# Performance work log

Hardware: AMD Instinct MI355X
Metric: run time of the kernel (lower is better)

## Reference

```python
import jax, jax.numpy as jnp
import numpy as np

LMAX = 6
F_IN, F_OUT = 64, 64
N_ROT = 64  # n_angles**3
IRREP_FLAT = sum((2 * l + 1) ** 2 for l in range(LMAX + 1))  # 455
BATCH = 1024


def setup_inputs() -> dict:
    key = jax.random.key(0)
    k_x, k_d, k_w = jax.random.split(key, 3)
    x = jax.random.normal(k_x, (BATCH, F_IN, IRREP_FLAT), dtype=jnp.float32)
    D = jax.random.normal(k_d, (N_ROT, IRREP_FLAT), dtype=jnp.float32)  # flat Wigner-D buffer
    w = jax.random.normal(k_w, (F_IN, F_OUT, N_ROT), dtype=jnp.float32)
    return {"x": x, "D": D, "w": w}


def reference(x, D, w):
    B, f_in, _ = x.shape
    f_out = w.shape[1]
    n_rot = D.shape[0]
    # psi[f,g,i] = sum_n D[n,i] * w[f,g,n] / sqrt(N)
    psi = jnp.einsum('ni,fgn->fgi', D, w) / jnp.sqrt(jnp.asarray(n_rot, x.dtype))
    outs = []
    off = 0
    for l in range(LMAX + 1):
        d = 2 * l + 1          # irrep dim == multiplicity for so3_irreps
        blk = d * d
        # weight block: (f_in, f_out, mul_in=u, mul_out=v)
        Wl = psi[:, :, off:off + blk].reshape(f_in, f_out, d, d)
        # input block: (B, f_in, mul=u, irrep_dim=m)
        xl = x[:, :, off:off + blk].reshape(B, f_in, d, d)
        # e3nn Linear path norm ('element'): 1/sqrt(f_in * mul_in)
        norm = 1.0 / np.sqrt(f_in * d)
        yl = jnp.einsum('bfum,fguv->bgvm', xl, Wl) * norm
        outs.append(yl.reshape(B, f_out, blk))
        off += blk
    return jnp.concatenate(outs, axis=-1)  # (B, f_out, 455)
```

## Files before the change

kernel.cpp:

```cpp
#include <hip/hip_runtime.h>
#include <stdint.h>


typedef __bf16 bf16x8 __attribute__((ext_vector_type(8)));
typedef float floatx4 __attribute__((ext_vector_type(4)));

#define XROW 29120

__device__ __forceinline__ unsigned short f2bf(float f) {
  union { float f; unsigned int u; } c; c.f = f;
  unsigned int u = c.u;
  return (unsigned short)((u + 0x7FFFu + ((u >> 16) & 1u)) >> 16);
}
__device__ __forceinline__ unsigned int pack2(float a, float b) {
  return (unsigned int)f2bf(a) | ((unsigned int)f2bf(b) << 16);
}

__host__ __device__ constexpr int d_of(int L) { return 2 * L + 1; }
__host__ __device__ constexpr int off_of(int L) { int s = 0; for (int i = 0; i < L; ++i) s += d_of(i) * d_of(i); return s; }
__host__ __device__ constexpr size_t a_off(int L) { size_t s = 0; for (int i = 0; i < L; ++i) s += (size_t)65536 * d_of(i) * d_of(i); return s; }
__host__ __device__ constexpr size_t b_off(int L) { size_t s = a_off(7); for (int i = 0; i < L; ++i) s += (size_t)4096 * d_of(i) * (d_of(i) + 1); return s; }

__global__ __launch_bounds__(256) void prep(const float* __restrict__ x, const float* __restrict__ Dm,
                                            const float* __restrict__ w, unsigned short* __restrict__ ws) {
  __shared__ __align__(16) float smem[64 * 68 + 64 * 172];
  const int tid = threadIdx.x;
  const int bid = blockIdx.x;

  if (bid < 448) {
    float* wg = smem;
    float* Dl = smem + 64 * 68;
    const int g = bid & 63, l = bid >> 6;
    const int d = 2 * l + 1, d2 = d * d, K = 64 * d;
    int off = 0; size_t boff = a_off(7);
    for (int i = 0; i < l; ++i) { int dd = 2 * i + 1; off += dd * dd; boff += (size_t)4096 * dd * (dd + 1); }
    unsigned short* B = ws + boff;

    for (int t = tid; t < 4096; t += 256) {
      int n = t & 63, f = t >> 6;
      wg[n * 68 + f] = w[(size_t)f * 4096 + g * 64 + n];
    }
    for (int t = tid; t < 64 * 172; t += 256) {
      int n = t / 172, r = t - n * 172;
      Dl[t] = (r < d2) ? Dm[n * 455 + off + r] : 0.f;
    }
    __syncthreads();

    const float sl = 1.0f / (64.0f * sqrtf((float)d));
    const int RT = (d2 + 3) >> 2;
    for (int tt = tid; tt < 16 * RT; tt += 256) {
      const int ft = tt & 15, rt = tt >> 4;
      float acc[4][4] = {};
      for (int n = 0; n < 64; ++n) {
        floatx4 wv = *(const floatx4*)(wg + n * 68 + ft * 4);
        floatx4 dv = *(const floatx4*)(Dl + n * 172 + rt * 4);
#pragma unroll
        for (int a = 0; a < 4; ++a)
#pragma unroll
          for (int b2 = 0; b2 < 4; ++b2) acc[a][b2] += wv[a] * dv[b2];
      }
#pragma unroll
      for (int b2 = 0; b2 < 4; ++b2) {
        int r = rt * 4 + b2;
        if (r < d2) {
          int u = r / d, v = r - u * d;
          size_t base = (size_t)(g * d + v) * K + u * 64 + ft * 4;
#pragma unroll
          for (int a = 0; a < 4; ++a) B[base + a] = f2bf(acc[a][b2] * sl);
        }
      }
    }
    {
      int nn = 64 * d + g;
      for (int k = tid; k < K; k += 256) B[(size_t)nn * K + k] = 0;
    }
  } else {
    float* xs = smem;
    const int b = bid - 448;
    const float* xb = x + (size_t)b * XROW;
    size_t aoff = 0;

    for (int t = tid; t < 64 * 165; t += 256) { int f = t / 165, c = t - f * 165; xs[t] = xb[(size_t)f * 455 + c]; }
    __syncthreads();
    int off = 0;
#pragma unroll
    for (int l = 0; l < 5; ++l) {
      const int d = 2 * l + 1, d2 = d * d, n1 = 64 * d2;
      unsigned int* A = (unsigned int*)(ws + aoff + (size_t)b * n1);
      for (int t = tid; t < (n1 >> 1); t += 256) {
        int f2 = t & 31, s = t >> 5;
        int u = s % d, m = s / d;
        int c = off + u * d + m;
        A[t] = pack2(xs[(2 * f2) * 165 + c], xs[(2 * f2 + 1) * 165 + c]);
      }
      off += d2; aoff += (size_t)1024 * n1;
    }
    __syncthreads();
    for (int t = tid; t < 64 * 121; t += 256) { int f = t / 121, c = t - f * 121; xs[t] = xb[(size_t)f * 455 + 165 + c]; }
    __syncthreads();
    {
      const int n1 = 64 * 121;
      unsigned int* A = (unsigned int*)(ws + aoff + (size_t)b * n1);
      for (int t = tid; t < (n1 >> 1); t += 256) {
        int f2 = t & 31, s = t >> 5;
        int u = s % 11, m = s / 11;
        int c = u * 11 + m;
        A[t] = pack2(xs[(2 * f2) * 121 + c], xs[(2 * f2 + 1) * 121 + c]);
      }
      aoff += (size_t)1024 * n1;
    }
    __syncthreads();
    for (int t = tid; t < 64 * 169; t += 256) { int f = t / 169, c = t - f * 169; xs[t] = xb[(size_t)f * 455 + 286 + c]; }
    __syncthreads();
    {
      const int n1 = 64 * 169;
      unsigned int* A = (unsigned int*)(ws + aoff + (size_t)b * n1);
      for (int t = tid; t < (n1 >> 1); t += 256) {
        int f2 = t & 31, s = t >> 5;
        int u = s % 13, m = s / 13;
        int c = u * 13 + m;
        A[t] = pack2(xs[(2 * f2) * 169 + c], xs[(2 * f2 + 1) * 169 + c]);
      }
    }
  }
}

__device__ __forceinline__ void async_copy16(const void* gp, void* lp) {
  __builtin_amdgcn_global_load_lds((__attribute__((address_space(1))) void*)gp,
                                   (__attribute__((address_space(3))) void*)lp, 16, 0, 0);
}

template <int L>
__device__ __forceinline__ void gemm_body(int local, const unsigned short* __restrict__ ws,
                                          float* __restrict__ out,
                                          unsigned short* As, unsigned short* Bs) {
  constexpr int d = 2 * L + 1;
  constexpr int K = 64 * d;
  constexpr int NT = (d + 1) / 2;
  constexpr int OFF = off_of(L);
  const unsigned short* A = ws + a_off(L);
  const unsigned short* B = ws + b_off(L);
  const int x8 = local & 7, tt = local >> 3;
  const int mt = (tt / NT) * 8 + x8;
  const int nt = tt % NT;
  const int tid = threadIdx.x;
  const int w = tid >> 6, ln = tid & 63;
  const int wm = w >> 1, wn = w & 1;
  const int q = ln >> 4, r16 = ln & 15;

  const unsigned short* gp[4];
  unsigned short* ldst[4];
#pragma unroll
  for (int i = 0; i < 4; ++i) {
    int c = i * 256 + tid;
    if (i < 2) {
      gp[i] = A + (size_t)(mt * 128 + (c >> 2)) * K + (c & 3) * 8;
      ldst[i] = As + (i * 256 + w * 64) * 8;
    } else {
      int c2 = c - 512;
      gp[i] = B + (size_t)(nt * 128 + (c2 >> 2)) * K + (c2 & 3) * 8;
      ldst[i] = Bs + ((i - 2) * 256 + w * 64) * 8;
    }
  }

  const int aoffs0 = (wm * 64 + r16) * 32 + q * 8;
  const int boffs0 = (wn * 64 + r16) * 32 + q * 8;

  floatx4 acc[4][4] = {};

  for (int kt = 0; kt < 2 * d; ++kt) {
    __syncthreads();
#pragma unroll
    for (int i = 0; i < 4; ++i) async_copy16(gp[i], ldst[i]);
    __syncthreads();
    bf16x8 af[4], bfr[4];
#pragma unroll
    for (int mi = 0; mi < 4; ++mi) af[mi] = *(const bf16x8*)(As + aoffs0 + mi * 512);
#pragma unroll
    for (int ni = 0; ni < 4; ++ni) bfr[ni] = *(const bf16x8*)(Bs + boffs0 + ni * 512);
#pragma unroll
    for (int mi = 0; mi < 4; ++mi)
#pragma unroll
      for (int ni = 0; ni < 4; ++ni)
        acc[mi][ni] = __builtin_amdgcn_mfma_f32_16x16x32_bf16(af[mi], bfr[ni], acc[mi][ni], 0, 0, 0);
#pragma unroll
    for (int i = 0; i < 4; ++i) gp[i] += 32;
  }

#pragma unroll
  for (int ni = 0; ni < 4; ++ni) {
    int Cc = nt * 128 + wn * 64 + ni * 16 + r16;
    if (Cc < 64 * d) {
      int g = Cc / d, v = Cc - (Cc / d) * d;
#pragma unroll
      for (int mi = 0; mi < 4; ++mi) {
        int R0 = mt * 128 + wm * 64 + mi * 16 + q * 4;
#pragma unroll
        for (int reg = 0; reg < 4; ++reg) {
          int R = R0 + reg;
          int bb = R / d, m = R - (R / d) * d;
          out[(size_t)bb * XROW + g * 455 + OFF + v * d + m] = acc[mi][ni][reg];
        }
      }
    }
  }
}

__global__ __launch_bounds__(256) void gemm_all(const unsigned short* __restrict__ ws, float* __restrict__ out) {
  __shared__ alignas(16) unsigned short As[128 * 32];
  __shared__ alignas(16) unsigned short Bs[128 * 32];
  int b0 = 2015 - (int)blockIdx.x;
  if      (b0 <    8) gemm_body<0>(b0,        ws, out, As, Bs);
  else if (b0 <   56) gemm_body<1>(b0 -    8, ws, out, As, Bs);
  else if (b0 <  176) gemm_body<2>(b0 -   56, ws, out, As, Bs);
  else if (b0 <  400) gemm_body<3>(b0 -  176, ws, out, As, Bs);
  else if (b0 <  760) gemm_body<4>(b0 -  400, ws, out, As, Bs);
  else if (b0 < 1288) gemm_body<5>(b0 -  760, ws, out, As, Bs);
  else                gemm_body<6>(b0 - 1288, ws, out, As, Bs);
}

extern "C" void kernel_launch(void* const* d_in, const int* in_sizes, int n_in,
                              void* d_out, int out_size, void* d_ws, size_t ws_size,
                              hipStream_t stream) {
  const float* x = (const float*)d_in[0];
  const float* D = (const float*)d_in[1];
  const float* w = (const float*)d_in[2];
  float* out = (float*)d_out;
  unsigned short* ws = (unsigned short*)d_ws;

  hipLaunchKernelGGL(prep, dim3(1472), dim3(256), 0, stream, x, D, w, ws);
  hipLaunchKernelGGL(gemm_all, dim3(2016), dim3(256), 0, stream, ws, out);
}
```

Before: 364.5 us.

## Double-buffer LDS tiles in grouped GEMM and XOR-swizzle LDS layout

The GEMM main loop now keeps two LDS buffers for A and B, issuing the async global-to-LDS copy for the next k-tile before computing on the current one, with a single barrier per iteration instead of two. The 16-byte chunk index within each 64-byte row is XOR-swizzled on both the load and the read side to reduce LDS bank conflicts on the bf16x8 fragment reads. This doubles LDS use per block, which may lower occupancy, and correctness depends on the async copies having completed when the single barrier is passed.

```diff
diff --git a/kernel.cpp b/kernel.cpp
--- a/kernel.cpp
+++ b/kernel.cpp
@@ -138,6 +138,7 @@
   constexpr int K = 64 * d;
   constexpr int NT = (d + 1) / 2;
   constexpr int OFF = off_of(L);
+  constexpr int KT = 2 * d;
   const unsigned short* A = ws + a_off(L);
   const unsigned short* B = ws + b_off(L);
   const int x8 = local & 7, tt = local >> 3;
@@ -154,37 +155,48 @@
   for (int i = 0; i < 4; ++i) {
     int c = i * 256 + tid;
     if (i < 2) {
-      gp[i] = A + (size_t)(mt * 128 + (c >> 2)) * K + (c & 3) * 8;
+      int row = c >> 2, ch = (c & 3) ^ ((c >> 3) & 3);
+      gp[i] = A + (size_t)(mt * 128 + row) * K + ch * 8;
       ldst[i] = As + (i * 256 + w * 64) * 8;
     } else {
       int c2 = c - 512;
-      gp[i] = B + (size_t)(nt * 128 + (c2 >> 2)) * K + (c2 & 3) * 8;
+      int row = c2 >> 2, ch = (c2 & 3) ^ ((c2 >> 3) & 3);
+      gp[i] = B + (size_t)(nt * 128 + row) * K + ch * 8;
       ldst[i] = Bs + ((i - 2) * 256 + w * 64) * 8;
     }
   }
 
-  const int aoffs0 = (wm * 64 + r16) * 32 + q * 8;
-  const int boffs0 = (wn * 64 + r16) * 32 + q * 8;
+  const int sq = q ^ ((r16 >> 1) & 3);
+  const int aoffs0 = (wm * 64 + r16) * 32 + sq * 8;
+  const int boffs0 = (wn * 64 + r16) * 32 + sq * 8;
 
   floatx4 acc[4][4] = {};
 
-  for (int kt = 0; kt < 2 * d; ++kt) {
-    __syncthreads();
-#pragma unroll
-    for (int i = 0; i < 4; ++i) async_copy16(gp[i], ldst[i]);
-    __syncthreads();
+#pragma unroll
+  for (int i = 0; i < 4; ++i) { async_copy16(gp[i], ldst[i]); gp[i] += 32; }
+  __syncthreads();
+
+  int cur = 0;
+  for (int kt = 0; kt < KT; ++kt) {
+    if (kt + 1 < KT) {
+      const int nb = (cur ^ 1) * 4096;
+#pragma unroll
+      for (int i = 0; i < 4; ++i) { async_copy16(gp[i], ldst[i] + nb); gp[i] += 32; }
+    }
+    const unsigned short* Asc = As + cur * 4096;
+    const unsigned short* Bsc = Bs + cur * 4096;
     bf16x8 af[4], bfr[4];
 #pragma unroll
-    for (int mi = 0; mi < 4; ++mi) af[mi] = *(const bf16x8*)(As + aoffs0 + mi * 512);
-#pragma unroll
-    for (int ni = 0; ni < 4; ++ni) bfr[ni] = *(const bf16x8*)(Bs + boffs0 + ni * 512);
+    for (int mi = 0; mi < 4; ++mi) af[mi] = *(const bf16x8*)(Asc + aoffs0 + mi * 512);
+#pragma unroll
+    for (int ni = 0; ni < 4; ++ni) bfr[ni] = *(const bf16x8*)(Bsc + boffs0 + ni * 512);
 #pragma unroll
     for (int mi = 0; mi < 4; ++mi)
 #pragma unroll
       for (int ni = 0; ni < 4; ++ni)
         acc[mi][ni] = __builtin_amdgcn_mfma_f32_16x16x32_bf16(af[mi], bfr[ni], acc[mi][ni], 0, 0, 0);
-#pragma unroll
-    for (int i = 0; i < 4; ++i) gp[i] += 32;
+    __syncthreads();
+    cur ^= 1;
   }
 
 #pragma unroll
@@ -207,8 +219,8 @@
 }
 
 __global__ __launch_bounds__(256) void gemm_all(const unsigned short* __restrict__ ws, float* __restrict__ out) {
-  __shared__ alignas(16) unsigned short As[128 * 32];
-  __shared__ alignas(16) unsigned short Bs[128 * 32];
+  __shared__ alignas(16) unsigned short As[2 * 128 * 32];
+  __shared__ alignas(16) unsigned short Bs[2 * 128 * 32];
   int b0 = 2015 - (int)blockIdx.x;
   if      (b0 <    8) gemm_body<0>(b0,        ws, out, As, Bs);
   else if (b0 <   56) gemm_body<1>(b0 -    8, ws, out, As, Bs);
```

Result: no change. 369.9 us (+1.5%).
